# Kernel tuning notes

Hardware: AMD Instinct MI355X
Metric: run time of the kernel (lower is better)

The kernel has to match this reference:

```python
import jax, jax.numpy as jnp
import numpy as np

B, S, E, H = 8, 2048, 384, 6
D = E // H  # head dim = 64


def setup_inputs() -> dict:
    key = jax.random.key(0)
    ks = jax.random.split(key, 5)
    s = 1.0 / np.sqrt(E)
    return {
        "x": jax.random.normal(ks[0], (B, S, E), dtype=jnp.float32),
        "Wq": jax.random.normal(ks[1], (E, E), dtype=jnp.float32) * s,
        "Wk": jax.random.normal(ks[2], (E, E), dtype=jnp.float32) * s,
        "Wv": jax.random.normal(ks[3], (E, E), dtype=jnp.float32) * s,
        "Wo": jax.random.normal(ks[4], (E, E), dtype=jnp.float32) * s,
        "bo": jnp.zeros((E,), dtype=jnp.float32),
    }


def reference(x, Wq, Wk, Wv, Wo, bo):
    b, s, e = x.shape
    # QKV projections (torch Linear with bias=False: x @ W.T; here W stored as [in,out])
    q = (x @ Wq).reshape(b, s, H, D).transpose(0, 2, 1, 3)  # [b,h,s,d]
    k = (x @ Wk).reshape(b, s, H, D).transpose(0, 2, 1, 3)
    v = (x @ Wv).reshape(b, s, H, D).transpose(0, 2, 1, 3)
    scores = jnp.einsum("bhqd,bhkd->bhqk", q, k) / jnp.sqrt(jnp.asarray(D, x.dtype))
    causal = jnp.tril(jnp.ones((s, s), dtype=bool))
    scores = jnp.where(causal, scores, -jnp.inf)
    attn = jax.nn.softmax(scores, axis=-1)
    # NOTE: original applies dropout but then uses the PRE-dropout softmax for @V,
    # so dropout is a no-op; we faithfully omit it.
    out = jnp.einsum("bhqk,bhkd->bhqd", attn, v)  # [b,h,s,d]
    out = out.transpose(0, 2, 1, 3).reshape(b, s, e)
    return out @ Wo + bo
```

## Files before the change

### kernel.cpp

```cpp
#include <hip/hip_runtime.h>
#include <hip/hip_bf16.h>
#include <cstdint>
#include <cstddef>

typedef __attribute__((ext_vector_type(8))) short short8;
typedef __attribute__((ext_vector_type(4))) float f32x4;

#define S_LEN 2048
#define EMB 384
#define NH 6
#define HD 64
#define NB 8
#define QSCALE 0.180336880f

__device__ __forceinline__ unsigned short f2bf(float f) {
  return __builtin_bit_cast(unsigned short, __float2bfloat16(f));
}

__global__ __launch_bounds__(256) void k_prepw(
    const float* __restrict__ Wq, const float* __restrict__ Wk,
    const float* __restrict__ Wv, const float* __restrict__ Wo,
    unsigned short* __restrict__ Wqt, unsigned short* __restrict__ Wkt,
    unsigned short* __restrict__ Wvt, unsigned short* __restrict__ Wot) {
  __shared__ unsigned short Lw[64 * 66];
  const int tid = threadIdx.x;
  const int bx2 = blockIdx.x;
  const int mat = bx2 / 36;
  const int tile = bx2 - mat * 36;
  const int k0 = (tile / 6) * 64;
  const int n0 = (tile % 6) * 64;
  const float* W = (mat == 0) ? Wq : (mat == 1) ? Wk : (mat == 2) ? Wv : Wo;
  unsigned short* Wt = (mat == 0) ? Wqt : (mat == 1) ? Wkt : (mat == 2) ? Wvt : Wot;
  const int f4 = tid & 15;
#pragma unroll
  for (int it = 0; it < 4; ++it) {
    const int kl = it * 16 + (tid >> 4);
    const float4 v = reinterpret_cast<const float4*>(W + (size_t)(k0 + kl) * EMB + n0)[f4];
    Lw[kl * 66 + f4 * 4 + 0] = f2bf(v.x);
    Lw[kl * 66 + f4 * 4 + 1] = f2bf(v.y);
    Lw[kl * 66 + f4 * 4 + 2] = f2bf(v.z);
    Lw[kl * 66 + f4 * 4 + 3] = f2bf(v.w);
  }
  __syncthreads();
  const int g = tid & 7;
#pragma unroll
  for (int it = 0; it < 2; ++it) {
    const int nl = it * 32 + (tid >> 3);
    short8 o;
#pragma unroll
    for (int j = 0; j < 8; ++j) o[j] = (short)Lw[(g * 8 + j) * 66 + nl];
    *reinterpret_cast<short8*>(Wt + (size_t)(n0 + nl) * EMB + k0 + g * 8) = o;
  }
}

__global__ __launch_bounds__(256) void k_qkv(
    const float* __restrict__ x,
    const unsigned short* __restrict__ Wqt,
    const unsigned short* __restrict__ Wkt,
    const unsigned short* __restrict__ Wvt,
    unsigned short* __restrict__ Qb,
    unsigned short* __restrict__ Kb,
    unsigned short* __restrict__ Vtb) {
  __shared__ __attribute__((aligned(16))) unsigned short La[128 * 72];
  __shared__ __attribute__((aligned(16))) unsigned short Lt[64 * 136];

  const int tid = threadIdx.x;
  const int lane = tid & 63;
  const int w = tid >> 6;
  const int wr = w >> 1, wc = w & 1;
  const int lr = lane & 15, lg = lane >> 4;

  const int bid = blockIdx.y * 128 + blockIdx.x;
  const int xcd = bid & 7;
  const int pos = bid >> 3;
  const int bx = xcd * 16 + (pos & 15);
  const int by = pos >> 4;
  const int m0 = bx * 128;
  const int wsel = by / 3;
  const int n0 = (by % 3) * 128;
  const unsigned short* Wt = (wsel == 0) ? Wqt : (wsel == 1) ? Wkt : Wvt;

  const int srow = tid >> 3;
  const int sg = tid & 7;

  f32x4 acc[4][4] = {};
  float4 xf[4][2];
  short8 breg[2][2][4];

#pragma unroll
  for (int i = 0; i < 4; ++i) {
    const float* src = x + (size_t)(m0 + i * 32 + srow) * EMB + sg * 8;
    xf[i][0] = *reinterpret_cast<const float4*>(src);
    xf[i][1] = *reinterpret_cast<const float4*>(src + 4);
  }
#pragma unroll
  for (int kk = 0; kk < 2; ++kk)
#pragma unroll
    for (int ns = 0; ns < 4; ++ns)
      breg[0][kk][ns] = *reinterpret_cast<const short8*>(
          Wt + (size_t)(n0 + wc * 64 + ns * 16 + lr) * EMB + kk * 32 + lg * 8);

#pragma unroll
  for (int kt = 0; kt < 6; ++kt) {
    const int cur = kt & 1, nxt = cur ^ 1;
    __syncthreads();
#pragma unroll
    for (int i = 0; i < 4; ++i) {
      short8 v;
      v[0] = (short)f2bf(xf[i][0].x); v[1] = (short)f2bf(xf[i][0].y);
      v[2] = (short)f2bf(xf[i][0].z); v[3] = (short)f2bf(xf[i][0].w);
      v[4] = (short)f2bf(xf[i][1].x); v[5] = (short)f2bf(xf[i][1].y);
      v[6] = (short)f2bf(xf[i][1].z); v[7] = (short)f2bf(xf[i][1].w);
      *reinterpret_cast<short8*>(&La[(i * 32 + srow) * 72 + sg * 8]) = v;
    }
    __syncthreads();
    if (kt < 5) {
      const int kn = (kt + 1) * 64;
#pragma unroll
      for (int i = 0; i < 4; ++i) {
        const float* src = x + (size_t)(m0 + i * 32 + srow) * EMB + kn + sg * 8;
        xf[i][0] = *reinterpret_cast<const float4*>(src);
        xf[i][1] = *reinterpret_cast<const float4*>(src + 4);
      }
#pragma unroll
      for (int kk = 0; kk < 2; ++kk)
#pragma unroll
        for (int ns = 0; ns < 4; ++ns)
          breg[nxt][kk][ns] = *reinterpret_cast<const short8*>(
              Wt + (size_t)(n0 + wc * 64 + ns * 16 + lr) * EMB + kn + kk * 32 + lg * 8);
    }
#pragma unroll
    for (int kk = 0; kk < 2; ++kk) {
      short8 a[4];
#pragma unroll
      for (int ms = 0; ms < 4; ++ms)
        a[ms] = *reinterpret_cast<const short8*>(
            &La[(wr * 64 + ms * 16 + lr) * 72 + kk * 32 + lg * 8]);
#pragma unroll
      for (int ms = 0; ms < 4; ++ms)
#pragma unroll
        for (int ns = 0; ns < 4; ++ns)
          acc[ms][ns] = __builtin_amdgcn_mfma_f32_16x16x32_bf16(
              a[ms], breg[cur][kk][ns], acc[ms][ns], 0, 0, 0);
    }
  }

  const int bb = m0 >> 11;
  const int s0 = m0 & 2047;
  if (wsel != 2) {
    unsigned short* Out = (wsel == 0) ? Qb : Kb;
    const float sc = (wsel == 0) ? QSCALE : 1.0f;
#pragma unroll
    for (int p = 0; p < 2; ++p) {
      __syncthreads();
      if (wr == p) {
#pragma unroll
        for (int ms = 0; ms < 4; ++ms)
#pragma unroll
          for (int ns = 0; ns < 4; ++ns)
#pragma unroll
            for (int r = 0; r < 4; ++r)
              Lt[(ms * 16 + lg * 4 + r) * 136 + wc * 64 + ns * 16 + lr] =
                  f2bf(acc[ms][ns][r] * sc);
      }
      __syncthreads();
#pragma unroll
      for (int it = 0; it < 4; ++it) {
        const int row = (tid >> 3) + 32 * (it & 1);
        const int ch = (tid & 7) + 8 * (it >> 1);
        const short8 v = *reinterpret_cast<const short8*>(&Lt[row * 136 + ch * 8]);
        const int n = n0 + ch * 8;
        const int h = n >> 6, d = n & 63;
        *reinterpret_cast<short8*>(
            Out + (((size_t)bb * NH + h) * S_LEN + (s0 + p * 64 + row)) * HD + d) = v;
      }
    }
  } else {
#pragma unroll
    for (int p = 0; p < 2; ++p) {
      __syncthreads();
      if (wc == p) {
#pragma unroll
        for (int ms = 0; ms < 4; ++ms)
#pragma unroll
          for (int ns = 0; ns < 4; ++ns)
#pragma unroll
            for (int r = 0; r < 4; ++r) {
              const int dl = ns * 16 + lr;
              const int ml = wr * 64 + ms * 16 + lg * 4 + r;
              Lt[dl * 136 + (((ml >> 3) ^ (dl & 7)) << 3) + (ml & 7)] = f2bf(acc[ms][ns][r]);
            }
      }
      __syncthreads();
      const int hg = 2 * (n0 >> 7) + p;
      const int c = tid & 15;
#pragma unroll
      for (int it = 0; it < 4; ++it) {
        const int d = it * 16 + (tid >> 4);
        const short8 v = *reinterpret_cast<const short8*>(
            &Lt[d * 136 + ((c ^ (d & 7)) << 3)]);
        *reinterpret_cast<short8*>(
            Vtb + (((size_t)bb * NH + hg) * HD + d) * S_LEN + s0 + c * 8) = v;
      }
    }
  }
}

__global__ __launch_bounds__(256) void k_attn(
    const unsigned short* __restrict__ Qb,
    const unsigned short* __restrict__ Kb,
    const unsigned short* __restrict__ Vtg,
    unsigned short* __restrict__ Ob) {
  __shared__ __attribute__((aligned(16))) unsigned short Ks[64 * 64];
  __shared__ __attribute__((aligned(16))) unsigned short Vt[64 * 64];
  __shared__ __attribute__((aligned(16))) unsigned short Ps[64 * 64];

  const int tid = threadIdx.x;
  const int lane = tid & 63;
  const int w = tid >> 6;
  const int lr = lane & 15, lg = lane >> 4;

  const int lin = blockIdx.y * 16 + blockIdx.x;
  const int swz = (lin & 7) * 96 + (lin >> 3);
  const int pair = swz & 15;
  const int bh = swz >> 4;

  const unsigned short* Qp = Qb + (size_t)bh * S_LEN * HD;
  const unsigned short* Kp = Kb + (size_t)bh * S_LEN * HD;
  const unsigned short* Vp = Vtg + (size_t)bh * S_LEN * HD;
  const int b = bh / NH, hh = bh - b * NH;

  const int srow = tid >> 3;
  const int sslot = tid & 7;
  const int wsl0 = (sslot ^ (srow & 7)) << 3;

  for (int phase = 0; phase < 2; ++phase) {
    const int qt = phase ? (31 - pair) : pair;
    const int qbase = qt * 64 + w * 16;

    const short8 aq0 = *reinterpret_cast<const short8*>(Qp + (size_t)(qbase + lr) * HD + lg * 8);
    const short8 aq1 = *reinterpret_cast<const short8*>(Qp + (size_t)(qbase + lr) * HD + 32 + lg * 8);

    f32x4 o[4] = {};
    float l_i[4] = {0.f, 0.f, 0.f, 0.f};

    short8 pk0 = *reinterpret_cast<const short8*>(Kp + (size_t)srow * HD + sslot * 8);
    short8 pk1 = *reinterpret_cast<const short8*>(Kp + (size_t)(srow + 32) * HD + sslot * 8);
    short8 pv0 = *reinterpret_cast<const short8*>(Vp + (size_t)srow * S_LEN + sslot * 8);
    short8 pv1 = *reinterpret_cast<const short8*>(Vp + (size_t)(srow + 32) * S_LEN + sslot * 8);

    for (int t = 0; t <= qt; ++t) {
      __syncthreads();
      *reinterpret_cast<short8*>(&Ks[srow * 64 + wsl0]) = pk0;
      *reinterpret_cast<short8*>(&Ks[(srow + 32) * 64 + wsl0]) = pk1;
      *reinterpret_cast<short8*>(&Vt[srow * 64 + wsl0]) = pv0;
      *reinterpret_cast<short8*>(&Vt[(srow + 32) * 64 + wsl0]) = pv1;
      __syncthreads();

      if (t < qt) {
        const int tn = (t + 1) * 64;
        pk0 = *reinterpret_cast<const short8*>(Kp + (size_t)(tn + srow) * HD + sslot * 8);
        pk1 = *reinterpret_cast<const short8*>(Kp + (size_t)(tn + srow + 32) * HD + sslot * 8);
        pv0 = *reinterpret_cast<const short8*>(Vp + (size_t)srow * S_LEN + tn + sslot * 8);
        pv1 = *reinterpret_cast<const short8*>(Vp + (size_t)(srow + 32) * S_LEN + tn + sslot * 8);
      }

      float sv[4][4];
#pragma unroll
      for (int ks = 0; ks < 4; ++ks) {
        const int kstart = t * 64 + ks * 16;
        if (kstart > qbase + 15) {
#pragma unroll
          for (int r = 0; r < 4; ++r) sv[ks][r] = -1e30f;
        } else {
          const int krow = ks * 16 + lr;
          const int kx = krow & 7;
          const short8 bk0 = *reinterpret_cast<const short8*>(&Ks[krow * 64 + ((lg ^ kx) << 3)]);
          const short8 bk1 = *reinterpret_cast<const short8*>(&Ks[krow * 64 + (((4 + lg) ^ kx) << 3)]);
          f32x4 s = {};
          s = __builtin_amdgcn_mfma_f32_16x16x32_bf16(aq0, bk0, s, 0, 0, 0);
          s = __builtin_amdgcn_mfma_f32_16x16x32_bf16(aq1, bk1, s, 0, 0, 0);
          if (kstart + 15 <= qbase) {
#pragma unroll
            for (int r = 0; r < 4; ++r) sv[ks][r] = s[r];
          } else {
            const int kg = kstart + lr;
#pragma unroll
            for (int r = 0; r < 4; ++r)
              sv[ks][r] = (kg <= qbase + lg * 4 + r) ? s[r] : -1e30f;
          }
        }
      }

#pragma unroll
      for (int r = 0; r < 4; ++r) {
        const int q = w * 16 + lg * 4 + r;
        const int qx = q & 7;
        const int abase = q * 64 + (lr & 7);
        const int sp = lr >> 3;
        float p[4];
#pragma unroll
        for (int ks = 0; ks < 4; ++ks) p[ks] = __builtin_amdgcn_exp2f(sv[ks][r]);
        l_i[r] += (p[0] + p[1]) + (p[2] + p[3]);
#pragma unroll
        for (int ks = 0; ks < 4; ++ks)
          Ps[abase + ((((ks << 1) | sp) ^ qx) << 3)] = f2bf(p[ks]);
      }

      const int qrow = w * 16 + lr;
      const int qx2 = qrow & 7;
#pragma unroll
      for (int kk = 0; kk < 2; ++kk) {
        const short8 ap = *reinterpret_cast<const short8*>(
            &Ps[qrow * 64 + (((kk * 4 + lg) ^ qx2) << 3)]);
#pragma unroll
        for (int ns = 0; ns < 4; ++ns) {
          const int vrow = ns * 16 + lr;
          const short8 bv = *reinterpret_cast<const short8*>(
              &Vt[vrow * 64 + (((kk * 4 + lg) ^ (vrow & 7)) << 3)]);
          o[ns] = __builtin_amdgcn_mfma_f32_16x16x32_bf16(ap, bv, o[ns], 0, 0, 0);
        }
      }
    }

#pragma unroll
    for (int r = 0; r < 4; ++r) {
      float l = l_i[r];
      l += __shfl_xor(l, 1);
      l += __shfl_xor(l, 2);
      l += __shfl_xor(l, 4);
      l += __shfl_xor(l, 8);
      l_i[r] = 1.0f / l;
    }
#pragma unroll
    for (int ns = 0; ns < 4; ++ns)
#pragma unroll
      for (int r = 0; r < 4; ++r) {
        const int qg = qbase + lg * 4 + r;
        const float val = o[ns][r] * l_i[r];
        Ob[((size_t)(b * S_LEN + qg)) * EMB + hh * HD + ns * 16 + lr] = f2bf(val);
      }
  }
}

__global__ __launch_bounds__(256) void k_oproj(
    const unsigned short* __restrict__ Ob,
    const unsigned short* __restrict__ Wot,
    const float* __restrict__ bo,
    float* __restrict__ out) {
  __shared__ __attribute__((aligned(16))) unsigned short La[64 * 72];
  __shared__ __attribute__((aligned(16))) float Lf[64 * 132];

  const int tid = threadIdx.x;
  const int lane = tid & 63;
  const int w = tid >> 6;
  const int lr = lane & 15, lg = lane >> 4;

  const int bid = blockIdx.y * 256 + blockIdx.x;
  const int xcd = bid & 7;
  const int pos = bid >> 3;
  const int m0 = (xcd * 32 + (pos & 31)) * 64;
  const int n0 = (pos >> 5) * 128;

  const int srow = tid >> 3;
  const int sg = tid & 7;

  f32x4 acc[4][2] = {};
  short8 st[2];
  short8 breg[2][2][2];

#pragma unroll
  for (int i = 0; i < 2; ++i)
    st[i] = *reinterpret_cast<const short8*>(
        Ob + (size_t)(m0 + i * 32 + srow) * EMB + sg * 8);
#pragma unroll
  for (int kk = 0; kk < 2; ++kk)
#pragma unroll
    for (int ns = 0; ns < 2; ++ns)
      breg[0][kk][ns] = *reinterpret_cast<const short8*>(
          Wot + (size_t)(n0 + w * 32 + ns * 16 + lr) * EMB + kk * 32 + lg * 8);

#pragma unroll
  for (int kt = 0; kt < 6; ++kt) {
    const int cur = kt & 1, nxt = cur ^ 1;
    __syncthreads();
#pragma unroll
    for (int i = 0; i < 2; ++i)
      *reinterpret_cast<short8*>(&La[(i * 32 + srow) * 72 + sg * 8]) = st[i];
    __syncthreads();
    if (kt < 5) {
      const int kn = (kt + 1) * 64;
#pragma unroll
      for (int i = 0; i < 2; ++i)
        st[i] = *reinterpret_cast<const short8*>(
            Ob + (size_t)(m0 + i * 32 + srow) * EMB + kn + sg * 8);
#pragma unroll
      for (int kk = 0; kk < 2; ++kk)
#pragma unroll
        for (int ns = 0; ns < 2; ++ns)
          breg[nxt][kk][ns] = *reinterpret_cast<const short8*>(
              Wot + (size_t)(n0 + w * 32 + ns * 16 + lr) * EMB + kn + kk * 32 + lg * 8);
    }
#pragma unroll
    for (int kk = 0; kk < 2; ++kk) {
      short8 a[4];
#pragma unroll
      for (int ms = 0; ms < 4; ++ms)
        a[ms] = *reinterpret_cast<const short8*>(
            &La[(ms * 16 + lr) * 72 + kk * 32 + lg * 8]);
#pragma unroll
      for (int ms = 0; ms < 4; ++ms)
#pragma unroll
        for (int ns = 0; ns < 2; ++ns)
          acc[ms][ns] = __builtin_amdgcn_mfma_f32_16x16x32_bf16(
              a[ms], breg[cur][kk][ns], acc[ms][ns], 0, 0, 0);
    }
  }

  __syncthreads();
#pragma unroll
  for (int ms = 0; ms < 4; ++ms)
#pragma unroll
    for (int ns = 0; ns < 2; ++ns)
#pragma unroll
      for (int r = 0; r < 4; ++r)
        Lf[(ms * 16 + lg * 4 + r) * 132 + w * 32 + ns * 16 + lr] = acc[ms][ns][r];
  __syncthreads();
#pragma unroll
  for (int it = 0; it < 8; ++it) {
    const int row = (tid >> 3) + 32 * (it & 1);
    const int c4 = (tid & 7) + 8 * (it >> 1);
    float4 v = *reinterpret_cast<const float4*>(&Lf[row * 132 + c4 * 4]);
    const float4 b4 = *reinterpret_cast<const float4*>(&bo[n0 + c4 * 4]);
    v.x += b4.x; v.y += b4.y; v.z += b4.z; v.w += b4.w;
    *reinterpret_cast<float4*>(&out[(size_t)(m0 + row) * EMB + n0 + c4 * 4]) = v;
  }
}

extern "C" void kernel_launch(void* const* d_in, const int* in_sizes, int n_in,
                              void* d_out, int out_size, void* d_ws, size_t ws_size,
                              hipStream_t stream) {
  const float* x  = (const float*)d_in[0];
  const float* Wq = (const float*)d_in[1];
  const float* Wk = (const float*)d_in[2];
  const float* Wv = (const float*)d_in[3];
  const float* Wo = (const float*)d_in[4];
  const float* bo = (const float*)d_in[5];
  float* out = (float*)d_out;

  uint8_t* ws = (uint8_t*)d_ws;
  unsigned short* Wqt = (unsigned short*)(ws + 12582912);
  unsigned short* Wkt = (unsigned short*)(ws + 12877824);
  unsigned short* Wvt = (unsigned short*)(ws + 13172736);
  unsigned short* Wot = (unsigned short*)(ws + 13467648);
  unsigned short* Qb  = (unsigned short*)(ws + 13762560);
  unsigned short* Kb  = (unsigned short*)(ws + 26345472);
  unsigned short* VT  = (unsigned short*)(ws + 38928384);
  unsigned short* Ob  = (unsigned short*)(ws + 51511296);

  hipLaunchKernelGGL(k_prepw, dim3(144), dim3(256), 0, stream,
                     Wq, Wk, Wv, Wo, Wqt, Wkt, Wvt, Wot);
  hipLaunchKernelGGL(k_qkv, dim3(128, 9), dim3(256), 0, stream,
                     x, Wqt, Wkt, Wvt, Qb, Kb, VT);
  hipLaunchKernelGGL(k_attn, dim3(16, 48), dim3(256), 0, stream, Qb, Kb, VT, Ob);
  hipLaunchKernelGGL(k_oproj, dim3(256, 3), dim3(256), 0, stream, Ob, Wot, bo, out);
}
```

Measured before the change: 202.2 us.

## Share K/V tiles across paired query tiles with double-buffered LDS in attention

The attention kernel now processes both query tiles of a causal pair (qt and 31-qt) in one pass over K/V, so each K/V tile is loaded into LDS once and used by both. K/V staging is double-buffered, which cuts one barrier per iteration and overlaps the next tile's global load with compute. Diagonal-tile work is trimmed by skipping fully masked QK and PV MFMAs. The block-to-pair mapping is reordered, and launch bounds request 3 blocks per CU. The cost is more registers for two sets of accumulators and double the LDS footprint, which may limit occupancy.

```diff
diff --git a/kernel.cpp b/kernel.cpp
--- a/kernel.cpp
+++ b/kernel.cpp
@@ -206,14 +206,85 @@
   }
 }
 
-__global__ __launch_bounds__(256) void k_attn(
+__device__ __forceinline__ void attn_step(
+    const unsigned short* __restrict__ K, const unsigned short* __restrict__ V,
+    unsigned short* __restrict__ Ps,
+    const short8 aq0, const short8 aq1,
+    const int t, const int qt, const int qbase,
+    const int w, const int lr, const int lg,
+    f32x4* o, float* l_i) {
+  const bool diag = (t == qt);
+  const int kkmax = diag ? ((w >> 1) + 1) : 2;
+  const int ksmax = kkmax * 2;
+
+  float sv[4][4];
+#pragma unroll
+  for (int ks = 0; ks < 4; ++ks) {
+    if (!diag || ks <= w) {
+      const int krow = ks * 16 + lr;
+      const int kx = krow & 7;
+      const short8 bk0 = *reinterpret_cast<const short8*>(&K[krow * 64 + ((lg ^ kx) << 3)]);
+      const short8 bk1 = *reinterpret_cast<const short8*>(&K[krow * 64 + (((4 + lg) ^ kx) << 3)]);
+      f32x4 s = {};
+      s = __builtin_amdgcn_mfma_f32_16x16x32_bf16(aq0, bk0, s, 0, 0, 0);
+      s = __builtin_amdgcn_mfma_f32_16x16x32_bf16(aq1, bk1, s, 0, 0, 0);
+      if (diag && ks == w) {
+#pragma unroll
+        for (int r = 0; r < 4; ++r)
+          sv[ks][r] = (lr <= lg * 4 + r) ? s[r] : -1e30f;
+      } else {
+#pragma unroll
+        for (int r = 0; r < 4; ++r) sv[ks][r] = s[r];
+      }
+    }
+  }
+
+#pragma unroll
+  for (int r = 0; r < 4; ++r) {
+    const int q = w * 16 + lg * 4 + r;
+    const int qx = q & 7;
+    const int abase = q * 64 + (lr & 7);
+    const int sp = lr >> 3;
+    float s = 0.f;
+#pragma unroll
+    for (int ks = 0; ks < 4; ++ks) {
+      if (!diag || ks <= w) {
+        const float p = __builtin_amdgcn_exp2f(sv[ks][r]);
+        s += p;
+        Ps[abase + ((((ks << 1) | sp) ^ qx) << 3)] = f2bf(p);
+      } else if (ks < ksmax) {
+        Ps[abase + ((((ks << 1) | sp) ^ qx) << 3)] = 0;
+      }
+    }
+    l_i[r] += s;
+  }
+
+  const int qrow = w * 16 + lr;
+  const int qx2 = qrow & 7;
+#pragma unroll
+  for (int kk = 0; kk < 2; ++kk) {
+    if (kk < kkmax) {
+      const short8 ap = *reinterpret_cast<const short8*>(
+          &Ps[qrow * 64 + (((kk * 4 + lg) ^ qx2) << 3)]);
+#pragma unroll
+      for (int ns = 0; ns < 4; ++ns) {
+        const int vrow = ns * 16 + lr;
+        const short8 bv = *reinterpret_cast<const short8*>(
+            &V[vrow * 64 + (((kk * 4 + lg) ^ (vrow & 7)) << 3)]);
+        o[ns] = __builtin_amdgcn_mfma_f32_16x16x32_bf16(ap, bv, o[ns], 0, 0, 0);
+      }
+    }
+  }
+}
+
+__global__ __launch_bounds__(256, 3) void k_attn(
     const unsigned short* __restrict__ Qb,
     const unsigned short* __restrict__ Kb,
     const unsigned short* __restrict__ Vtg,
     unsigned short* __restrict__ Ob) {
-  __shared__ __attribute__((aligned(16))) unsigned short Ks[64 * 64];
-  __shared__ __attribute__((aligned(16))) unsigned short Vt[64 * 64];
-  __shared__ __attribute__((aligned(16))) unsigned short Ps[64 * 64];
+  __shared__ __attribute__((aligned(16))) unsigned short Ksb[2][64 * 64];
+  __shared__ __attribute__((aligned(16))) unsigned short Vtb[2][64 * 64];
+  __shared__ __attribute__((aligned(16))) unsigned short Psb[2][64 * 64];
 
   const int tid = threadIdx.x;
   const int lane = tid & 63;
@@ -222,8 +293,10 @@
 
   const int lin = blockIdx.y * 16 + blockIdx.x;
   const int swz = (lin & 7) * 96 + (lin >> 3);
-  const int pair = swz & 15;
+  const int idx = swz & 15;
   const int bh = swz >> 4;
+  const int pair = (idx & 1) ? (15 - (idx >> 1)) : (idx >> 1);
+  const int qtA = pair, qtB = 31 - pair;
 
   const unsigned short* Qp = Qb + (size_t)bh * S_LEN * HD;
   const unsigned short* Kp = Kb + (size_t)bh * S_LEN * HD;
@@ -234,113 +307,70 @@
   const int sslot = tid & 7;
   const int wsl0 = (sslot ^ (srow & 7)) << 3;
 
-  for (int phase = 0; phase < 2; ++phase) {
-    const int qt = phase ? (31 - pair) : pair;
-    const int qbase = qt * 64 + w * 16;
-
-    const short8 aq0 = *reinterpret_cast<const short8*>(Qp + (size_t)(qbase + lr) * HD + lg * 8);
-    const short8 aq1 = *reinterpret_cast<const short8*>(Qp + (size_t)(qbase + lr) * HD + 32 + lg * 8);
-
-    f32x4 o[4] = {};
-    float l_i[4] = {0.f, 0.f, 0.f, 0.f};
-
-    short8 pk0 = *reinterpret_cast<const short8*>(Kp + (size_t)srow * HD + sslot * 8);
-    short8 pk1 = *reinterpret_cast<const short8*>(Kp + (size_t)(srow + 32) * HD + sslot * 8);
-    short8 pv0 = *reinterpret_cast<const short8*>(Vp + (size_t)srow * S_LEN + sslot * 8);
-    short8 pv1 = *reinterpret_cast<const short8*>(Vp + (size_t)(srow + 32) * S_LEN + sslot * 8);
-
-    for (int t = 0; t <= qt; ++t) {
-      __syncthreads();
-      *reinterpret_cast<short8*>(&Ks[srow * 64 + wsl0]) = pk0;
-      *reinterpret_cast<short8*>(&Ks[(srow + 32) * 64 + wsl0]) = pk1;
-      *reinterpret_cast<short8*>(&Vt[srow * 64 + wsl0]) = pv0;
-      *reinterpret_cast<short8*>(&Vt[(srow + 32) * 64 + wsl0]) = pv1;
-      __syncthreads();
-
-      if (t < qt) {
-        const int tn = (t + 1) * 64;
-        pk0 = *reinterpret_cast<const short8*>(Kp + (size_t)(tn + srow) * HD + sslot * 8);
-        pk1 = *reinterpret_cast<const short8*>(Kp + (size_t)(tn + srow + 32) * HD + sslot * 8);
-        pv0 = *reinterpret_cast<const short8*>(Vp + (size_t)srow * S_LEN + tn + sslot * 8);
-        pv1 = *reinterpret_cast<const short8*>(Vp + (size_t)(srow + 32) * S_LEN + tn + sslot * 8);
-      }
-
-      float sv[4][4];
-#pragma unroll
-      for (int ks = 0; ks < 4; ++ks) {
-        const int kstart = t * 64 + ks * 16;
-        if (kstart > qbase + 15) {
-#pragma unroll
-          for (int r = 0; r < 4; ++r) sv[ks][r] = -1e30f;
-        } else {
-          const int krow = ks * 16 + lr;
-          const int kx = krow & 7;
-          const short8 bk0 = *reinterpret_cast<const short8*>(&Ks[krow * 64 + ((lg ^ kx) << 3)]);
-          const short8 bk1 = *reinterpret_cast<const short8*>(&Ks[krow * 64 + (((4 + lg) ^ kx) << 3)]);
-          f32x4 s = {};
-          s = __builtin_amdgcn_mfma_f32_16x16x32_bf16(aq0, bk0, s, 0, 0, 0);
-          s = __builtin_amdgcn_mfma_f32_16x16x32_bf16(aq1, bk1, s, 0, 0, 0);
-          if (kstart + 15 <= qbase) {
-#pragma unroll
-            for (int r = 0; r < 4; ++r) sv[ks][r] = s[r];
-          } else {
-            const int kg = kstart + lr;
-#pragma unroll
-            for (int r = 0; r < 4; ++r)
-              sv[ks][r] = (kg <= qbase + lg * 4 + r) ? s[r] : -1e30f;
-          }
-        }
-      }
-
-#pragma unroll
-      for (int r = 0; r < 4; ++r) {
-        const int q = w * 16 + lg * 4 + r;
-        const int qx = q & 7;
-        const int abase = q * 64 + (lr & 7);
-        const int sp = lr >> 3;
-        float p[4];
-#pragma unroll
-        for (int ks = 0; ks < 4; ++ks) p[ks] = __builtin_amdgcn_exp2f(sv[ks][r]);
-        l_i[r] += (p[0] + p[1]) + (p[2] + p[3]);
-#pragma unroll
-        for (int ks = 0; ks < 4; ++ks)
-          Ps[abase + ((((ks << 1) | sp) ^ qx) << 3)] = f2bf(p[ks]);
-      }
-
-      const int qrow = w * 16 + lr;
-      const int qx2 = qrow & 7;
-#pragma unroll
-      for (int kk = 0; kk < 2; ++kk) {
-        const short8 ap = *reinterpret_cast<const short8*>(
-            &Ps[qrow * 64 + (((kk * 4 + lg) ^ qx2) << 3)]);
-#pragma unroll
-        for (int ns = 0; ns < 4; ++ns) {
-          const int vrow = ns * 16 + lr;
-          const short8 bv = *reinterpret_cast<const short8*>(
-              &Vt[vrow * 64 + (((kk * 4 + lg) ^ (vrow & 7)) << 3)]);
-          o[ns] = __builtin_amdgcn_mfma_f32_16x16x32_bf16(ap, bv, o[ns], 0, 0, 0);
-        }
-      }
-    }
-
+  const int qbA = qtA * 64 + w * 16;
+  const int qbB = qtB * 64 + w * 16;
+
+  const short8 aqA0 = *reinterpret_cast<const short8*>(Qp + (size_t)(qbA + lr) * HD + lg * 8);
+  const short8 aqA1 = *reinterpret_cast<const short8*>(Qp + (size_t)(qbA + lr) * HD + 32 + lg * 8);
+  const short8 aqB0 = *reinterpret_cast<const short8*>(Qp + (size_t)(qbB + lr) * HD + lg * 8);
+  const short8 aqB1 = *reinterpret_cast<const short8*>(Qp + (size_t)(qbB + lr) * HD + 32 + lg * 8);
+
+  f32x4 oA[4] = {}, oB[4] = {};
+  float lA[4] = {0.f, 0.f, 0.f, 0.f}, lB[4] = {0.f, 0.f, 0.f, 0.f};
+
+  short8 pk0 = *reinterpret_cast<const short8*>(Kp + (size_t)srow * HD + sslot * 8);
+  short8 pk1 = *reinterpret_cast<const short8*>(Kp + (size_t)(srow + 32) * HD + sslot * 8);
+  short8 pv0 = *reinterpret_cast<const short8*>(Vp + (size_t)srow * S_LEN + sslot * 8);
+  short8 pv1 = *reinterpret_cast<const short8*>(Vp + (size_t)(srow + 32) * S_LEN + sslot * 8);
+  *reinterpret_cast<short8*>(&Ksb[0][srow * 64 + wsl0]) = pk0;
+  *reinterpret_cast<short8*>(&Ksb[0][(srow + 32) * 64 + wsl0]) = pk1;
+  *reinterpret_cast<short8*>(&Vtb[0][srow * 64 + wsl0]) = pv0;
+  *reinterpret_cast<short8*>(&Vtb[0][(srow + 32) * 64 + wsl0]) = pv1;
+  __syncthreads();
+
+  for (int t = 0; t <= qtB; ++t) {
+    const int cur = t & 1;
+    const bool more = t < qtB;
+    if (more) {
+      const int tn = (t + 1) * 64;
+      pk0 = *reinterpret_cast<const short8*>(Kp + (size_t)(tn + srow) * HD + sslot * 8);
+      pk1 = *reinterpret_cast<const short8*>(Kp + (size_t)(tn + srow + 32) * HD + sslot * 8);
+      pv0 = *reinterpret_cast<const short8*>(Vp + (size_t)srow * S_LEN + tn + sslot * 8);
+      pv1 = *reinterpret_cast<const short8*>(Vp + (size_t)(srow + 32) * S_LEN + tn + sslot * 8);
+    }
+
+    attn_step(Ksb[cur], Vtb[cur], Psb[1], aqB0, aqB1, t, qtB, qbB, w, lr, lg, oB, lB);
+    if (t <= qtA)
+      attn_step(Ksb[cur], Vtb[cur], Psb[0], aqA0, aqA1, t, qtA, qbA, w, lr, lg, oA, lA);
+
+    if (more) {
+      const int nxt = cur ^ 1;
+      *reinterpret_cast<short8*>(&Ksb[nxt][srow * 64 + wsl0]) = pk0;
+      *reinterpret_cast<short8*>(&Ksb[nxt][(srow + 32) * 64 + wsl0]) = pk1;
+      *reinterpret_cast<short8*>(&Vtb[nxt][srow * 64 + wsl0]) = pv0;
+      *reinterpret_cast<short8*>(&Vtb[nxt][(srow + 32) * 64 + wsl0]) = pv1;
+    }
+    __syncthreads();
+  }
+
+#pragma unroll
+  for (int r = 0; r < 4; ++r) {
+    float la = lA[r], lb = lB[r];
+    la += __shfl_xor(la, 1); lb += __shfl_xor(lb, 1);
+    la += __shfl_xor(la, 2); lb += __shfl_xor(lb, 2);
+    la += __shfl_xor(la, 4); lb += __shfl_xor(lb, 4);
+    la += __shfl_xor(la, 8); lb += __shfl_xor(lb, 8);
+    lA[r] = 1.0f / la; lB[r] = 1.0f / lb;
+  }
+#pragma unroll
+  for (int ns = 0; ns < 4; ++ns)
 #pragma unroll
     for (int r = 0; r < 4; ++r) {
-      float l = l_i[r];
-      l += __shfl_xor(l, 1);
-      l += __shfl_xor(l, 2);
-      l += __shfl_xor(l, 4);
-      l += __shfl_xor(l, 8);
-      l_i[r] = 1.0f / l;
-    }
-#pragma unroll
-    for (int ns = 0; ns < 4; ++ns)
-#pragma unroll
-      for (int r = 0; r < 4; ++r) {
-        const int qg = qbase + lg * 4 + r;
-        const float val = o[ns][r] * l_i[r];
-        Ob[((size_t)(b * S_LEN + qg)) * EMB + hh * HD + ns * 16 + lr] = f2bf(val);
-      }
-  }
+      const int qgA = qbA + lg * 4 + r;
+      const int qgB = qbB + lg * 4 + r;
+      Ob[((size_t)(b * S_LEN + qgA)) * EMB + hh * HD + ns * 16 + lr] = f2bf(oA[ns][r] * lA[r]);
+      Ob[((size_t)(b * S_LEN + qgB)) * EMB + hh * HD + ns * 16 + lr] = f2bf(oB[ns][r] * lB[r]);
+    }
 }
 
 __global__ __launch_bounds__(256) void k_oproj(
```

Result: faster. 191.1 us (-5.5%).
